# Kernel tuning notes

Measured on AMD Instinct MI355X. Metric: run time of the kernel, lower is better.

The kernel has to match this reference:

```python
import jax, jax.numpy as jnp
import numpy as np
import math

D_MODEL = 2048
NUM_HEADS = 16
D_K = D_MODEL // NUM_HEADS  # 128
THETA = 10000.0
BATCH = 2
SEQ = 2048


def setup_inputs() -> dict:
    key = jax.random.key(0)
    k1, k2, k3 = jax.random.split(key, 3)
    std_qkv = math.sqrt(2.0 / (D_MODEL + 3 * D_MODEL))
    std_o = math.sqrt(2.0 / (D_MODEL + D_MODEL))
    return {
        "x": jax.random.normal(k1, (BATCH, SEQ, D_MODEL), dtype=jnp.float32),
        "token_positions": jnp.arange(SEQ, dtype=jnp.int64 if jax.config.jax_enable_x64 else jnp.int32),
        "Wqkv": jax.random.normal(k2, (3 * D_MODEL, D_MODEL), dtype=jnp.float32) * std_qkv,
        "Wo": jax.random.normal(k3, (D_MODEL, D_MODEL), dtype=jnp.float32) * std_o,
    }


def _rope(x, positions):
    # x: [b, h, t, d_k]; interleaved even/odd rotation as in the torch module
    half = D_K // 2
    inv_freq = 1.0 / (THETA ** (jnp.arange(half, dtype=x.dtype) / half))
    ang = positions.astype(x.dtype)[:, None] * inv_freq[None, :]  # [t, half]
    sin, cos = jnp.sin(ang), jnp.cos(ang)                          # broadcast over b,h
    x_even, x_odd = x[..., 0::2], x[..., 1::2]
    rot_even = x_even * cos - x_odd * sin
    rot_odd = x_even * sin + x_odd * cos
    return jnp.stack([rot_even, rot_odd], axis=-1).reshape(x.shape)


def reference(x, token_positions, Wqkv, Wo):
    B, T, _ = x.shape
    qkv = x @ Wqkv.T                                  # [b, t, 3*d_model]
    q, k, v = jnp.split(qkv, 3, axis=-1)
    def to_heads(t):
        return t.reshape(B, T, NUM_HEADS, D_K).transpose(0, 2, 1, 3)  # b h t d
    q, k, v = to_heads(q), to_heads(k), to_heads(v)
    q = _rope(q, token_positions)
    k = _rope(k, token_positions)
    scale = 1.0 / math.sqrt(D_K)
    scores = jnp.einsum("bhqd,bhkd->bhqk", q, k) * scale
    causal = jnp.tril(jnp.ones((T, T), dtype=bool))
    scores = jnp.where(causal, scores, jnp.finfo(scores.dtype).min)
    attn = jax.nn.softmax(scores, axis=-1)
    out = jnp.einsum("bhqk,bhkd->bhqd", attn, v)
    out = out.transpose(0, 2, 1, 3).reshape(B, T, D_MODEL)
    return out @ Wo.T
```

## Files before the change

### kernel.cpp

```cpp
#include <hip/hip_runtime.h>
#include <math.h>
#include <stdint.h>

#define NHEADS 16
#define DK 128
#define TSEQ 2048
#define DMODEL 2048

typedef __attribute__((ext_vector_type(8))) short short8;
typedef __attribute__((ext_vector_type(4))) float floatx4;

__device__ __forceinline__ float bf2f(unsigned short h) {
    return __uint_as_float(((unsigned int)h) << 16);
}
__device__ __forceinline__ unsigned short f2bf(float f) {
    unsigned int u = __float_as_uint(f);
    u += 0x7FFFu + ((u >> 16) & 1u);
    return (unsigned short)(u >> 16);
}
__device__ __forceinline__ void async16(unsigned short* lds, const unsigned short* g) {
    __builtin_amdgcn_global_load_lds(
        (const __attribute__((address_space(1))) uint32_t*)g,
        (__attribute__((address_space(3))) uint32_t*)lds, 16, 0, 0);
}

#define NX8 1048576
#define NW8 1572864
#define NO8 524288
__global__ __launch_bounds__(256) void cast_all_bf16(
    const float* __restrict__ x, const float* __restrict__ wqkv, const float* __restrict__ wo,
    unsigned short* __restrict__ xb, unsigned short* __restrict__ wqkvb, unsigned short* __restrict__ wob)
{
    const int i = blockIdx.x * 256 + threadIdx.x;
    const float* src; unsigned short* dst; int k;
    if (i < NX8)            { src = x;    dst = xb;    k = i; }
    else if (i < NX8 + NW8) { src = wqkv; dst = wqkvb; k = i - NX8; }
    else                    { src = wo;   dst = wob;   k = i - NX8 - NW8; }
    const float4* p4 = reinterpret_cast<const float4*>(src) + 2 * (size_t)k;
    const float4 a = p4[0], b = p4[1];
    uint32_t w0 = (uint32_t)f2bf(a.x) | ((uint32_t)f2bf(a.y) << 16);
    uint32_t w1 = (uint32_t)f2bf(a.z) | ((uint32_t)f2bf(a.w) << 16);
    uint32_t w2 = (uint32_t)f2bf(b.x) | ((uint32_t)f2bf(b.y) << 16);
    uint32_t w3 = (uint32_t)f2bf(b.z) | ((uint32_t)f2bf(b.w) << 16);
    uint4 o; o.x = w0; o.y = w1; o.z = w2; o.w = w3;
    *reinterpret_cast<uint4*>(dst + 8 * (size_t)k) = o;
}

__global__ __launch_bounds__(256) void rope_table_kernel(
    const int* __restrict__ pos, float2* __restrict__ tab)
{
    const int idx = blockIdx.x * 256 + threadIdx.x;
    const int tt = idx >> 6, i = idx & 63;
    const double inv_freq = exp(-log(10000.0) * (double)i / 64.0);
    const double ang = (double)pos[tt] * inv_freq;
    tab[idx] = make_float2((float)cos(ang), (float)sin(ang));
}

__global__ __launch_bounds__(256, 2) void gemm_qkv_x(
    const unsigned short* __restrict__ A, const unsigned short* __restrict__ B,
    unsigned short* __restrict__ qkvb, unsigned short* __restrict__ vt,
    const float2* __restrict__ tab)
{
    const int K = DMODEL, N = 3 * DMODEL;
    __shared__ unsigned short As[2][128 * 64];
    __shared__ unsigned short Bs[2][192 * 64];

    const int t = threadIdx.x;
    const int lane = t & 63, w = t >> 6;
    const int wr = w >> 1, wc = w & 1;
    const int lr = lane & 15, hi = lane >> 4;

    const int bid = (int)blockIdx.x;
    const int xcd = bid & 7, local = bid >> 3;
    const int row0 = (local & 31) * 128;
    const int col0 = ((xcd << 2) | (local >> 5)) * 192;

    const int rr = t >> 3;
    const int cc = ((t & 7) ^ (rr & 7)) << 3;
    const unsigned short* aP = A + (size_t)(row0 + rr) * K + cc;
    const unsigned short* bP = B + (size_t)(col0 + rr) * K + cc;
    const size_t rstep = (size_t)32 * K;

    floatx4 acc[4][6];
#pragma unroll
    for (int m = 0; m < 4; m++)
#pragma unroll
        for (int n = 0; n < 6; n++)
#pragma unroll
            for (int e = 0; e < 4; e++) acc[m][n][e] = 0.f;

#define STAGE(nb, k0n) do { \
        async16(&As[nb][t * 8],          aP + (k0n)); \
        async16(&As[nb][(t + 256) * 8],  aP + rstep + (k0n)); \
        async16(&As[nb][(t + 512) * 8],  aP + 2 * rstep + (k0n)); \
        async16(&As[nb][(t + 768) * 8],  aP + 3 * rstep + (k0n)); \
        async16(&Bs[nb][t * 8],          bP + (k0n)); \
        async16(&Bs[nb][(t + 256) * 8],  bP + rstep + (k0n)); \
        async16(&Bs[nb][(t + 512) * 8],  bP + 2 * rstep + (k0n)); \
        async16(&Bs[nb][(t + 768) * 8],  bP + 3 * rstep + (k0n)); \
        async16(&Bs[nb][(t + 1024) * 8], bP + 4 * rstep + (k0n)); \
        async16(&Bs[nb][(t + 1280) * 8], bP + 5 * rstep + (k0n)); \
    } while (0)

    const int NT = K >> 6;
    const int ch0 = (hi ^ (lr & 7)) * 8;
    const int ch1 = ((4 + hi) ^ (lr & 7)) * 8;

    short8 av[4], bv[6];

#define RD_AV(Ac, ch) do { \
        _Pragma("unroll") \
        for (int m = 0; m < 4; m++) \
            av[m] = *(const short8*)&(Ac)[(wr * 64 + m * 16 + lr) * 64 + (ch)]; \
    } while (0)
#define RD_BV(Bc, ch) do { \
        _Pragma("unroll") \
        for (int n = 0; n < 6; n++) \
            bv[n] = *(const short8*)&(Bc)[(wc * 96 + n * 16 + lr) * 64 + (ch)]; \
    } while (0)
#define MFMA_ALL() do { \
        _Pragma("unroll") \
        for (int m = 0; m < 4; m++) \
            _Pragma("unroll") \
            for (int n = 0; n < 6; n++) \
                acc[m][n] = __builtin_amdgcn_mfma_f32_16x16x32_bf16(av[m], bv[n], acc[m][n], 0, 0, 0); \
    } while (0)

    STAGE(0, 0);

    for (int kt = 0; kt < NT; ++kt) {
        const int cur = kt & 1;
        const unsigned short* __restrict__ Ac = &As[cur][0];
        const unsigned short* __restrict__ Bc = &Bs[cur][0];
        const bool more = (kt + 1 < NT);

        if (more) {
            STAGE(cur ^ 1, (kt + 1) << 6);
            asm volatile("s_waitcnt vmcnt(10)" ::: "memory");
        } else {
            asm volatile("s_waitcnt vmcnt(0)" ::: "memory");
        }
        __builtin_amdgcn_s_barrier();

        RD_AV(Ac, ch0); RD_BV(Bc, ch0);
        asm volatile("s_waitcnt lgkmcnt(0)" ::: "memory");
        __builtin_amdgcn_sched_barrier(0);
        __builtin_amdgcn_s_setprio(1);
        MFMA_ALL();
        __builtin_amdgcn_s_setprio(0);

        RD_AV(Ac, ch1); RD_BV(Bc, ch1);
        asm volatile("s_waitcnt lgkmcnt(0)" ::: "memory");
        __builtin_amdgcn_sched_barrier(0);
        __builtin_amdgcn_s_setprio(1);
        MFMA_ALL();
        __builtin_amdgcn_s_setprio(0);

        __builtin_amdgcn_s_barrier();
    }
#undef STAGE
#undef RD_AV
#undef RD_BV
#undef MFMA_ALL

    const int par = lr & 1;
#pragma unroll
    for (int mi = 0; mi < 4; mi++) {
        const int row = row0 + wr * 64 + mi * 16 + hi * 4;
        const int tt = row & (TSEQ - 1);
        const int bb = row >> 11;
#pragma unroll
        for (int ni = 0; ni < 6; ni++) {
            const int col = col0 + wc * 96 + ni * 16 + lr;
            if (col < 2 * DMODEL) {
                const int pi = (col & 127) >> 1;
#pragma unroll
                for (int j = 0; j < 4; j++) {
                    const float2 cs = tab[(tt + j) * 64 + pi];
                    const float v = acc[mi][ni][j];
                    const float p = __shfl_xor(v, 1, 64);
                    const float o = par ? (p * cs.y + v * cs.x)
                                        : (v * cs.x - p * cs.y);
                    qkvb[(size_t)(row + j) * N + col] = f2bf(o);
                }
            } else {
                const int vcol = col - 2 * DMODEL;
                const int h = vcol >> 7, d = vcol & 127;
                uint2 pw;
                pw.x = (uint32_t)f2bf(acc[mi][ni][0]) | ((uint32_t)f2bf(acc[mi][ni][1]) << 16);
                pw.y = (uint32_t)f2bf(acc[mi][ni][2]) | ((uint32_t)f2bf(acc[mi][ni][3]) << 16);
                *(uint2*)&vt[(size_t)((bb * NHEADS + h) * DK + d) * TSEQ + tt] = pw;
            }
        }
    }
}

__global__ __launch_bounds__(256, 2) void gemm_o_x(
    const unsigned short* __restrict__ A, const unsigned short* __restrict__ B,
    float* __restrict__ C)
{
    const int K = DMODEL, N = DMODEL;
    __shared__ unsigned short As[2][128 * 64];
    __shared__ unsigned short Bs[2][128 * 64];

    const int t = threadIdx.x;
    const int lane = t & 63, w = t >> 6;
    const int wr = w >> 1, wc = w & 1;
    const int lr = lane & 15, hi = lane >> 4;

    const int bid = (int)blockIdx.x;
    const int xcd = bid & 7, local = bid >> 3;
    const int row0 = (local & 31) * 128;
    const int col0 = ((xcd << 1) | (local >> 5)) * 128;

    const int rr = t >> 3;
    const int cc = ((t & 7) ^ (rr & 7)) << 3;
    const unsigned short* aP = A + (size_t)(row0 + rr) * K + cc;
    const unsigned short* bP = B + (size_t)(col0 + rr) * K + cc;
    const size_t rstep = (size_t)32 * K;

    floatx4 acc[4][4];
#pragma unroll
    for (int m = 0; m < 4; m++)
#pragma unroll
        for (int n = 0; n < 4; n++)
#pragma unroll
            for (int e = 0; e < 4; e++) acc[m][n][e] = 0.f;

#define STAGE(nb, k0n) do { \
        async16(&As[nb][t * 8],          aP + (k0n)); \
        async16(&As[nb][(t + 256) * 8],  aP + rstep + (k0n)); \
        async16(&As[nb][(t + 512) * 8],  aP + 2 * rstep + (k0n)); \
        async16(&As[nb][(t + 768) * 8],  aP + 3 * rstep + (k0n)); \
        async16(&Bs[nb][t * 8],          bP + (k0n)); \
        async16(&Bs[nb][(t + 256) * 8],  bP + rstep + (k0n)); \
        async16(&Bs[nb][(t + 512) * 8],  bP + 2 * rstep + (k0n)); \
        async16(&Bs[nb][(t + 768) * 8],  bP + 3 * rstep + (k0n)); \
    } while (0)

    const int NT = K >> 6;
    const int ch0 = (hi ^ (lr & 7)) * 8;
    const int ch1 = ((4 + hi) ^ (lr & 7)) * 8;

    short8 av[4], bv[4];

#define RD_AV(Ac, ch) do { \
        _Pragma("unroll") \
        for (int m = 0; m < 4; m++) \
            av[m] = *(const short8*)&(Ac)[(wr * 64 + m * 16 + lr) * 64 + (ch)]; \
    } while (0)
#define RD_BV(Bc, ch) do { \
        _Pragma("unroll") \
        for (int n = 0; n < 4; n++) \
            bv[n] = *(const short8*)&(Bc)[(wc * 64 + n * 16 + lr) * 64 + (ch)]; \
    } while (0)
#define MFMA_ALL() do { \
        _Pragma("unroll") \
        for (int m = 0; m < 4; m++) \
            _Pragma("unroll") \
            for (int n = 0; n < 4; n++) \
                acc[m][n] = __builtin_amdgcn_mfma_f32_16x16x32_bf16(av[m], bv[n], acc[m][n], 0, 0, 0); \
    } while (0)

    STAGE(0, 0);

    for (int kt = 0; kt < NT; ++kt) {
        const int cur = kt & 1;
        const unsigned short* __restrict__ Ac = &As[cur][0];
        const unsigned short* __restrict__ Bc = &Bs[cur][0];
        const bool more = (kt + 1 < NT);

        if (more) {
            STAGE(cur ^ 1, (kt + 1) << 6);
            asm volatile("s_waitcnt vmcnt(8)" ::: "memory");
        } else {
            asm volatile("s_waitcnt vmcnt(0)" ::: "memory");
        }
        __builtin_amdgcn_s_barrier();

        RD_AV(Ac, ch0); RD_BV(Bc, ch0);
        asm volatile("s_waitcnt lgkmcnt(0)" ::: "memory");
        __builtin_amdgcn_sched_barrier(0);
        __builtin_amdgcn_s_setprio(1);
        MFMA_ALL();
        __builtin_amdgcn_s_setprio(0);

        RD_AV(Ac, ch1); RD_BV(Bc, ch1);
        asm volatile("s_waitcnt lgkmcnt(0)" ::: "memory");
        __builtin_amdgcn_sched_barrier(0);
        __builtin_amdgcn_s_setprio(1);
        MFMA_ALL();
        __builtin_amdgcn_s_setprio(0);

        __builtin_amdgcn_s_barrier();
    }
#undef STAGE
#undef RD_AV
#undef RD_BV
#undef MFMA_ALL

#pragma unroll
    for (int mi = 0; mi < 4; mi++) {
        const int row = row0 + wr * 64 + mi * 16 + hi * 4;
#pragma unroll
        for (int ni = 0; ni < 4; ni++) {
            const int col = col0 + wc * 64 + ni * 16 + lr;
#pragma unroll
            for (int j = 0; j < 4; j++)
                C[(size_t)(row + j) * N + col] = acc[mi][ni][j];
        }
    }
}

__global__ __launch_bounds__(512, 1) void attn_mfma4_kernel(
    const unsigned short* __restrict__ qkvb, const unsigned short* __restrict__ vt,
    unsigned short* __restrict__ outb)
{
    __shared__ unsigned short Ks[2][64 * 128];
    __shared__ unsigned short Vs[2][128 * 64];
    __shared__ unsigned short Ps[8][32 * 64];

    const int t = threadIdx.x;
    const int lane = t & 63, w = t >> 6;
    const int lr = lane & 15, hi = lane >> 4;
    const int bh = (int)blockIdx.x & 31;
    const int p  = (int)blockIdx.x >> 5;
    const int b = bh >> 4, h = bh & 15;
    const int chunk = (w < 4) ? p : (15 - p);
    const int q0w = chunk * 128 + (w & 3) * 32;
    const float scale = 0.08838834764831845f;
    const size_t QROW = 3 * DMODEL;

    const unsigned short* kg = qkvb + (size_t)b * TSEQ * QROW + DMODEL + h * DK;
    const unsigned short* vg = vt + (size_t)bh * DK * TSEQ;

    short8 qf[2][4];
    {
        const unsigned short* qbase = qkvb + (size_t)(b * TSEQ + q0w) * QROW + h * DK;
#pragma unroll
        for (int nt = 0; nt < 2; nt++)
#pragma unroll
            for (int ks = 0; ks < 4; ks++) {
                short8 raw = *(const short8*)(qbase + (size_t)(nt * 16 + lr) * QROW + ks * 32 + hi * 8);
                short8 sc;
#pragma unroll
                for (int e = 0; e < 8; e++)
                    sc[e] = (short)f2bf(bf2f((unsigned short)raw[e]) * scale);
                qf[nt][ks] = sc;
            }
    }

    auto stageK = [&](int bufi, int kv0s) {
#pragma unroll
        for (int i = 0; i < 2; i++) {
            const int s = i * 512 + t;
            const int r = s >> 4;
            const int cc = (s & 15) ^ (r & 7);
            async16(&Ks[bufi][s * 8], kg + (size_t)(kv0s + r) * QROW + cc * 8);
        }
    };
    auto stageV = [&](int bufi, int kv0s) {
#pragma unroll
        for (int i = 0; i < 2; i++) {
            const int s = i * 512 + t;
            const int r = s >> 3;
            const int cc = (s & 7) ^ (r & 7);
            async16(&Vs[bufi][s * 8], vg + (size_t)r * TSEQ + kv0s + cc * 8);
        }
    };

    floatx4 accO[2][8];
#pragma unroll
    for (int nt = 0; nt < 2; nt++)
#pragma unroll
        for (int dt = 0; dt < 8; dt++)
#pragma unroll
            for (int e = 0; e < 4; e++) accO[nt][dt][e] = 0.f;
    float mrun[2] = {-1e30f, -1e30f};
    float lrun[2] = {0.f, 0.f};

    const int ntiles = (16 - p) * 2;
    int buf = 0;

    stageK(0, 0);
    stageV(0, 0);
    asm volatile("s_waitcnt vmcnt(0)" ::: "memory");
    __builtin_amdgcn_s_barrier();

    const int pswz = (lr & 7) << 1;

    for (int ti = 0; ti < ntiles; ti++) {
        const int kv0 = ti * 64;
        if (ti + 1 < ntiles) {
            stageK(buf ^ 1, kv0 + 64);
            stageV(buf ^ 1, kv0 + 64);
        }

        const bool active = (kv0 <= q0w + 31);

        if (active) {
            float al[2] = {1.f, 1.f};
            floatx4 st[4][2];
#pragma unroll
            for (int mt = 0; mt < 4; mt++)
#pragma unroll
                for (int nt = 0; nt < 2; nt++)
#pragma unroll
                    for (int e = 0; e < 4; e++) st[mt][nt][e] = 0.f;
#pragma unroll
            for (int mt = 0; mt < 4; mt++) {
                const int r = mt * 16 + lr;
#pragma unroll
                for (int ks = 0; ks < 4; ks++) {
                    const int ch = (ks * 4 + hi) ^ (r & 7);
                    const short8 kf = *(const short8*)&Ks[buf][(r * 16 + ch) * 8];
                    st[mt][0] = __builtin_amdgcn_mfma_f32_16x16x32_bf16(kf, qf[0][ks], st[mt][0], 0, 0, 0);
                    st[mt][1] = __builtin_amdgcn_mfma_f32_16x16x32_bf16(kf, qf[1][ks], st[mt][1], 0, 0, 0);
                }
            }
            if (kv0 + 63 > q0w) {
#pragma unroll
                for (int nt = 0; nt < 2; nt++) {
                    const int qg = q0w + nt * 16 + lr;
#pragma unroll
                    for (int mt = 0; mt < 4; mt++)
#pragma unroll
                        for (int rg = 0; rg < 4; rg++) {
                            const int kvg = kv0 + mt * 16 + hi * 4 + rg;
                            if (kvg > qg) st[mt][nt][rg] = -1e30f;
                        }
                }
            }
            float pm[2];
#pragma unroll
            for (int nt = 0; nt < 2; nt++) {
                float m = -1e30f;
#pragma unroll
                for (int mt = 0; mt < 4; mt++)
#pragma unroll
                    for (int rg = 0; rg < 4; rg++) m = fmaxf(m, st[mt][nt][rg]);
                m = fmaxf(m, __shfl_xor(m, 16, 64));
                m = fmaxf(m, __shfl_xor(m, 32, 64));
                pm[nt] = m;
            }
            if (__any((pm[0] > mrun[0] + 8.f) || (pm[1] > mrun[1] + 8.f))) {
#pragma unroll
                for (int nt = 0; nt < 2; nt++) {
                    const float mn = fmaxf(mrun[nt], pm[nt]);
                    al[nt] = __expf(mrun[nt] - mn);
                    mrun[nt] = mn;
                }
#pragma unroll
                for (int rg = 0; rg < 4; rg++) {
                    const float a0 = __shfl(al[0], hi * 4 + rg, 64);
                    const float a1 = __shfl(al[1], hi * 4 + rg, 64);
#pragma unroll
                    for (int dt = 0; dt < 8; dt++) {
                        accO[0][dt][rg] *= a0;
                        accO[1][dt][rg] *= a1;
                    }
                }
            }
#pragma unroll
            for (int nt = 0; nt < 2; nt++) {
                float ls = 0.f;
                const int prow = nt * 16 + lr;
#pragma unroll
                for (int mt = 0; mt < 4; mt++) {
                    float pv[4];
#pragma unroll
                    for (int rg = 0; rg < 4; rg++) {
                        pv[rg] = __expf(st[mt][nt][rg] - mrun[nt]);
                        ls += pv[rg];
                    }
                    uint2 pw;
                    pw.x = (uint32_t)f2bf(pv[0]) | ((uint32_t)f2bf(pv[1]) << 16);
                    pw.y = (uint32_t)f2bf(pv[2]) | ((uint32_t)f2bf(pv[3]) << 16);
                    const int chunkx = (mt * 4 + hi) ^ pswz;
                    *(uint2*)&Ps[w][prow * 64 + chunkx * 4] = pw;
                }
                ls += __shfl_xor(ls, 16, 64);
                ls += __shfl_xor(ls, 32, 64);
                lrun[nt] = lrun[nt] * al[nt] + ls;
            }

#pragma unroll
            for (int ks2 = 0; ks2 < 2; ks2++) {
                const int chp = ((ks2 * 8 + hi * 2) ^ pswz) * 4;
                const short8 pa0 = *(const short8*)&Ps[w][(0 * 16 + lr) * 64 + chp];
                const short8 pa1 = *(const short8*)&Ps[w][(1 * 16 + lr) * 64 + chp];
#pragma unroll
                for (int dt = 0; dt < 8; dt++) {
                    const int r = dt * 16 + lr;
                    const int ch = (ks2 * 4 + hi) ^ (r & 7);
                    const short8 vf = *(const short8*)&Vs[buf][(r * 8 + ch) * 8];
                    accO[0][dt] = __builtin_amdgcn_mfma_f32_16x16x32_bf16(pa0, vf, accO[0][dt], 0, 0, 0);
                    accO[1][dt] = __builtin_amdgcn_mfma_f32_16x16x32_bf16(pa1, vf, accO[1][dt], 0, 0, 0);
                }
            }
        }

        asm volatile("s_waitcnt vmcnt(0)" ::: "memory");
        __builtin_amdgcn_s_barrier();
        buf ^= 1;
    }

#pragma unroll
    for (int nt = 0; nt < 2; nt++) {
        const float lv_own = 1.f / lrun[nt];
#pragma unroll
        for (int rg = 0; rg < 4; rg++) {
            const float lv = __shfl(lv_own, hi * 4 + rg, 64);
            unsigned short* orow = outb + (size_t)(b * TSEQ + q0w + nt * 16 + hi * 4 + rg) * DMODEL + h * DK;
#pragma unroll
            for (int dt = 0; dt < 8; dt++)
                orow[dt * 16 + lr] = f2bf(accO[nt][dt][rg] * lv);
        }
    }
}

extern "C" void kernel_launch(void* const* d_in, const int* in_sizes, int n_in,
                              void* d_out, int out_size, void* d_ws, size_t ws_size,
                              hipStream_t stream)
{
    const float* x    = (const float*)d_in[0];
    const int*   pos  = (const int*)d_in[1];
    const float* Wqkv = (const float*)d_in[2];
    const float* Wo   = (const float*)d_in[3];
    float* out = (float*)d_out;

    unsigned short* qkvb  = (unsigned short*)d_ws;
    unsigned short* vtb   = qkvb + (size_t)25165824;
    unsigned short* xb    = vtb + (size_t)8388608;
    unsigned short* attnb = xb;
    unsigned short* wqkvb = xb + (size_t)8388608;
    unsigned short* wob   = wqkvb + (size_t)12582912;
    float2* tab = (float2*)(wob + (size_t)4194304);

    cast_all_bf16<<<12288, 256, 0, stream>>>(x, Wqkv, Wo, xb, wqkvb, wob);
    rope_table_kernel<<<512, 256, 0, stream>>>(pos, tab);

    gemm_qkv_x<<<dim3(1024), 256, 0, stream>>>(xb, wqkvb, qkvb, vtb, tab);

    attn_mfma4_kernel<<<dim3(256), 512, 0, stream>>>(qkvb, vtb, attnb);

    gemm_o_x<<<dim3(512), 256, 0, stream>>>(attnb, wob, out);
}
```

Before: 256.8 us.

## Fuse cast with rope table and split attention blocks into smaller two-per-CU blocks

The rope table computation is folded into the bf16 cast kernel, removing one launch. The attention kernel moves from 256 blocks of 512 threads to 512 blocks of 256 threads. Each block now handles half of a paired causal chunk (64 query rows per chunk), and two blocks can share a CU. This gives the scheduler finer work units, but each K/V tile is now staged from global memory by twice as many blocks, which adds load traffic.

```diff
diff --git a/kernel.cpp b/kernel.cpp
--- a/kernel.cpp
+++ b/kernel.cpp
@@ -27,33 +27,34 @@
 #define NX8 1048576
 #define NW8 1572864
 #define NO8 524288
-__global__ __launch_bounds__(256) void cast_all_bf16(
+#define NCAST (NX8 + NW8 + NO8)
+__global__ __launch_bounds__(256) void cast_rope_kernel(
     const float* __restrict__ x, const float* __restrict__ wqkv, const float* __restrict__ wo,
-    unsigned short* __restrict__ xb, unsigned short* __restrict__ wqkvb, unsigned short* __restrict__ wob)
+    const int* __restrict__ pos,
+    unsigned short* __restrict__ xb, unsigned short* __restrict__ wqkvb,
+    unsigned short* __restrict__ wob, float2* __restrict__ tab)
 {
     const int i = blockIdx.x * 256 + threadIdx.x;
-    const float* src; unsigned short* dst; int k;
-    if (i < NX8)            { src = x;    dst = xb;    k = i; }
-    else if (i < NX8 + NW8) { src = wqkv; dst = wqkvb; k = i - NX8; }
-    else                    { src = wo;   dst = wob;   k = i - NX8 - NW8; }
-    const float4* p4 = reinterpret_cast<const float4*>(src) + 2 * (size_t)k;
-    const float4 a = p4[0], b = p4[1];
-    uint32_t w0 = (uint32_t)f2bf(a.x) | ((uint32_t)f2bf(a.y) << 16);
-    uint32_t w1 = (uint32_t)f2bf(a.z) | ((uint32_t)f2bf(a.w) << 16);
-    uint32_t w2 = (uint32_t)f2bf(b.x) | ((uint32_t)f2bf(b.y) << 16);
-    uint32_t w3 = (uint32_t)f2bf(b.z) | ((uint32_t)f2bf(b.w) << 16);
-    uint4 o; o.x = w0; o.y = w1; o.z = w2; o.w = w3;
-    *reinterpret_cast<uint4*>(dst + 8 * (size_t)k) = o;
-}
-
-__global__ __launch_bounds__(256) void rope_table_kernel(
-    const int* __restrict__ pos, float2* __restrict__ tab)
-{
-    const int idx = blockIdx.x * 256 + threadIdx.x;
-    const int tt = idx >> 6, i = idx & 63;
-    const double inv_freq = exp(-log(10000.0) * (double)i / 64.0);
-    const double ang = (double)pos[tt] * inv_freq;
-    tab[idx] = make_float2((float)cos(ang), (float)sin(ang));
+    if (i < NCAST) {
+        const float* src; unsigned short* dst; int k;
+        if (i < NX8)            { src = x;    dst = xb;    k = i; }
+        else if (i < NX8 + NW8) { src = wqkv; dst = wqkvb; k = i - NX8; }
+        else                    { src = wo;   dst = wob;   k = i - NX8 - NW8; }
+        const float4* p4 = reinterpret_cast<const float4*>(src) + 2 * (size_t)k;
+        const float4 a = p4[0], b = p4[1];
+        uint32_t w0 = (uint32_t)f2bf(a.x) | ((uint32_t)f2bf(a.y) << 16);
+        uint32_t w1 = (uint32_t)f2bf(a.z) | ((uint32_t)f2bf(a.w) << 16);
+        uint32_t w2 = (uint32_t)f2bf(b.x) | ((uint32_t)f2bf(b.y) << 16);
+        uint32_t w3 = (uint32_t)f2bf(b.z) | ((uint32_t)f2bf(b.w) << 16);
+        uint4 o; o.x = w0; o.y = w1; o.z = w2; o.w = w3;
+        *reinterpret_cast<uint4*>(dst + 8 * (size_t)k) = o;
+    } else {
+        const int idx = i - NCAST;
+        const int tt = idx >> 6, pi = idx & 63;
+        const double inv_freq = exp(-log(10000.0) * (double)pi / 64.0);
+        const double ang = (double)pos[tt] * inv_freq;
+        tab[idx] = make_float2((float)cos(ang), (float)sin(ang));
+    }
 }
 
 __global__ __launch_bounds__(256, 2) void gemm_qkv_x(
@@ -312,22 +313,25 @@
     }
 }
 
-__global__ __launch_bounds__(512, 1) void attn_mfma4_kernel(
+__global__ __launch_bounds__(256, 2) void attn_mfma5_kernel(
     const unsigned short* __restrict__ qkvb, const unsigned short* __restrict__ vt,
     unsigned short* __restrict__ outb)
 {
     __shared__ unsigned short Ks[2][64 * 128];
     __shared__ unsigned short Vs[2][128 * 64];
-    __shared__ unsigned short Ps[8][32 * 64];
+    __shared__ unsigned short Ps[4][32 * 64];
 
     const int t = threadIdx.x;
     const int lane = t & 63, w = t >> 6;
     const int lr = lane & 15, hi = lane >> 4;
-    const int bh = (int)blockIdx.x & 31;
-    const int p  = (int)blockIdx.x >> 5;
+    const int bid  = (int)blockIdx.x;
+    const int bh   = bid & 31;
+    const int rest = bid >> 5;
+    const int p    = rest >> 1;
+    const int half = rest & 1;
     const int b = bh >> 4, h = bh & 15;
-    const int chunk = (w < 4) ? p : (15 - p);
-    const int q0w = chunk * 128 + (w & 3) * 32;
+    const int chunk = (w < 2) ? p : (15 - p);
+    const int q0w = chunk * 128 + half * 64 + (w & 1) * 32;
     const float scale = 0.08838834764831845f;
     const size_t QROW = 3 * DMODEL;
 
@@ -352,8 +356,8 @@
 
     auto stageK = [&](int bufi, int kv0s) {
 #pragma unroll
-        for (int i = 0; i < 2; i++) {
-            const int s = i * 512 + t;
+        for (int i = 0; i < 4; i++) {
+            const int s = i * 256 + t;
             const int r = s >> 4;
             const int cc = (s & 15) ^ (r & 7);
             async16(&Ks[bufi][s * 8], kg + (size_t)(kv0s + r) * QROW + cc * 8);
@@ -361,8 +365,8 @@
     };
     auto stageV = [&](int bufi, int kv0s) {
 #pragma unroll
-        for (int i = 0; i < 2; i++) {
-            const int s = i * 512 + t;
+        for (int i = 0; i < 4; i++) {
+            const int s = i * 256 + t;
             const int r = s >> 3;
             const int cc = (s & 7) ^ (r & 7);
             async16(&Vs[bufi][s * 8], vg + (size_t)r * TSEQ + kv0s + cc * 8);
@@ -537,12 +541,11 @@
     unsigned short* wob   = wqkvb + (size_t)12582912;
     float2* tab = (float2*)(wob + (size_t)4194304);
 
-    cast_all_bf16<<<12288, 256, 0, stream>>>(x, Wqkv, Wo, xb, wqkvb, wob);
-    rope_table_kernel<<<512, 256, 0, stream>>>(pos, tab);
+    cast_rope_kernel<<<12800, 256, 0, stream>>>(x, Wqkv, Wo, pos, xb, wqkvb, wob, tab);
 
     gemm_qkv_x<<<dim3(1024), 256, 0, stream>>>(xb, wqkvb, qkvb, vtb, tab);
 
-    attn_mfma4_kernel<<<dim3(256), 512, 0, stream>>>(qkvb, vtb, attnb);
+    attn_mfma5_kernel<<<dim3(512), 256, 0, stream>>>(qkvb, vtb, attnb);
 
     gemm_o_x<<<dim3(512), 256, 0, stream>>>(attnb, wob, out);
 }
```

Result: no change. 254.8 us (-0.8%).
